# Kernel optimization log

Hardware: AMD Instinct MI355X
Metric: run time of the kernel (lower is better)

## Reference

```python
import jax, jax.numpy as jnp
import numpy as np

L = 3          # num_layers
D = 512        # hidden_dim
B, N = 8, 1024
EPS = 1e-5


def layernorm(x, gamma, beta):
    mu = jnp.mean(x, axis=-1, keepdims=True)
    var = jnp.var(x, axis=-1, keepdims=True)
    return (x - mu) * jax.lax.rsqrt(var + EPS) * gamma + beta


def setup_inputs() -> dict:
    key = jax.random.key(0)
    ks = jax.random.split(key, 12)
    s = 1.0 / np.sqrt(D)
    node_features = jax.random.normal(ks[0], (B, N, D), dtype=jnp.float32)
    adjacency_matrix = jax.random.randint(ks[1], (B, N, N), 0, 2, dtype=jnp.int32)
    return {
        "node_features": node_features,
        "adjacency_matrix": adjacency_matrix,
        # attn_linear: Linear(2D, 1) -> weight [2D], bias scalar, per layer
        "attn_w": jax.random.normal(ks[2], (L, 2 * D), dtype=jnp.float32) * (1.0 / np.sqrt(2 * D)),
        "attn_b": jax.random.normal(ks[3], (L,), dtype=jnp.float32) * 0.01,
        "W1": jax.random.normal(ks[4], (L, D, 4 * D), dtype=jnp.float32) * s,
        "b1": jnp.zeros((L, 4 * D), dtype=jnp.float32),
        "W2": jax.random.normal(ks[5], (L, 4 * D, D), dtype=jnp.float32) * (1.0 / np.sqrt(4 * D)),
        "b2": jnp.zeros((L, D), dtype=jnp.float32),
        "g1": jnp.ones((L, D), dtype=jnp.float32),
        "beta1": jnp.zeros((L, D), dtype=jnp.float32),
        "g2": jnp.ones((L, D), dtype=jnp.float32),
        "beta2": jnp.zeros((L, D), dtype=jnp.float32),
    }


def reference(node_features, adjacency_matrix, attn_w, attn_b, W1, b1, W2, b2, g1, beta1, g2, beta2):
    n = adjacency_matrix.shape[-1]
    # adjacency + self loops; mask of allowed edges
    mask = (adjacency_matrix.astype(jnp.float32) + jnp.eye(n, dtype=jnp.float32)) > 0  # [B,N,N]
    x = node_features
    d = x.shape[-1]
    for l in range(attn_w.shape[0]):
        # score_ij = a1.h_i + a2.h_j + b  (== Linear(concat(h_i,h_j)))
        si = x @ attn_w[l, :d]           # [B,N]
        sj = x @ attn_w[l, d:]           # [B,N]
        scores = si[:, :, None] + sj[:, None, :] + attn_b[l]   # [B,N,N]
        scores = jnp.where(scores >= 0, scores, 0.2 * scores)  # LeakyReLU(0.2)
        scores = jnp.where(mask, scores, -jnp.inf)
        attn = jax.nn.softmax(scores, axis=-1)                  # diag always unmasked
        agg = jnp.einsum('bij,bjd->bid', attn, x)
        h = layernorm(x + agg, g1[l], beta1[l])
        ff = jax.nn.gelu(h @ W1[l] + b1[l], approximate=False) @ W2[l] + b2[l]
        x = layernorm(h + ff, g2[l], beta2[l])
    return x
```

## Files before the change

### kernel.cpp

```cpp
#include <hip/hip_runtime.h>
#include <math.h>

#define NB 8
#define NN 1024
#define DD 512

typedef unsigned short u16;
typedef unsigned int u32;
typedef unsigned long long u64;
typedef __attribute__((ext_vector_type(8))) short bfrag;
typedef __attribute__((ext_vector_type(4))) float ffrag;

__device__ __forceinline__ u16 f2b(float f) {
    union { float f; u32 u; } v; v.f = f;
    u32 r = v.u + 0x7fffu + ((v.u >> 16) & 1u);
    return (u16)(r >> 16);
}
__device__ __forceinline__ float b2f(u16 b) {
    union { u32 u; float f; } v; v.u = ((u32)b) << 16;
    return v.f;
}

__device__ __forceinline__ float gelu_cheap(float v) {
    float s = v * 0.70710678118654752f;
    float a = fabsf(s);
    float t = 1.0f / (1.0f + 0.3275911f * a);
    float p = ((((1.061405429f * t - 1.453152027f) * t + 1.421413741f) * t
                - 0.284496736f) * t + 0.254829592f) * t;
    float erfa = 1.0f - p * __expf(-a * a);
    float erfs = copysignf(erfa, s);
    return 0.5f * v * (1.0f + erfs);
}

__device__ __forceinline__ void gload_lds16(const void* g, void* l) {
    __builtin_amdgcn_global_load_lds(
        (const __attribute__((address_space(1))) void*)g,
        (__attribute__((address_space(3))) void*)l, 16, 0, 0);
}

__global__ __launch_bounds__(256) void mask_pack(const int* __restrict__ adj,
                                                 u64* __restrict__ mb) {
    int idx = blockIdx.x * 256 + threadIdx.x;
    int w = idx & 15;
    int bi = idx >> 4;
    int i = bi & 1023;
    const int4* p = (const int4*)(adj + (size_t)bi * NN + w * 64);
    u64 m = 0;
#pragma unroll
    for (int q = 0; q < 16; ++q) {
        int4 v = p[q];
        if (v.x > 0) m |= 1ull << (q * 4 + 0);
        if (v.y > 0) m |= 1ull << (q * 4 + 1);
        if (v.z > 0) m |= 1ull << (q * 4 + 2);
        if (v.w > 0) m |= 1ull << (q * 4 + 3);
    }
    if (w == (i >> 6)) m |= 1ull << (i & 63);
    mb[idx] = m;
}

__global__ __launch_bounds__(256) void transpose_cvt(
    const float* __restrict__ in, u16* __restrict__ out,
    int R, int C, size_t inStr, size_t outStr)
{
    __shared__ float tile[32][33];
    int z = blockIdx.z;
    int r0 = blockIdx.y * 32, c0 = blockIdx.x * 32;
    int t = threadIdx.x;
    int tr = t >> 3, tc = (t & 7) * 4;
    float4 v = *(const float4*)(in + inStr * z + (size_t)(r0 + tr) * C + c0 + tc);
    tile[tr][tc + 0] = v.x; tile[tr][tc + 1] = v.y;
    tile[tr][tc + 2] = v.z; tile[tr][tc + 3] = v.w;
    __syncthreads();
    u32 w0 = (u32)f2b(tile[tc + 0][tr]) | ((u32)f2b(tile[tc + 1][tr]) << 16);
    u32 w1 = (u32)f2b(tile[tc + 2][tr]) | ((u32)f2b(tile[tc + 3][tr]) << 16);
    uint2 wv; wv.x = w0; wv.y = w1;
    *(uint2*)(out + outStr * z + (size_t)(c0 + tr) * R + r0 + tc) = wv;
}

__global__ __launch_bounds__(256) void score_proj_kernel(
    const float* __restrict__ x, const float* __restrict__ w,
    float* __restrict__ si, float* __restrict__ sj)
{
    int wave = threadIdx.x >> 6;
    int lane = threadIdx.x & 63;
    int row = blockIdx.x * 4 + wave;
    const float4* xr = (const float4*)(x + (size_t)row * DD) + lane * 2;
    const float4* w1 = (const float4*)(w) + lane * 2;
    const float4* w2 = (const float4*)(w + DD) + lane * 2;
    float a = 0.f, b2 = 0.f;
#pragma unroll
    for (int c = 0; c < 2; ++c) {
        float4 xv = xr[c], wa = w1[c], wb = w2[c];
        a  += xv.x * wa.x + xv.y * wa.y + xv.z * wa.z + xv.w * wa.w;
        b2 += xv.x * wb.x + xv.y * wb.y + xv.z * wb.z + xv.w * wb.w;
    }
#pragma unroll
    for (int off = 32; off > 0; off >>= 1) {
        a  += __shfl_xor(a, off);
        b2 += __shfl_xor(b2, off);
    }
    if (lane == 0) { si[row] = a; sj[row] = b2; }
}

__global__ __launch_bounds__(256) void softmax_p(
    const float* __restrict__ si, const float* __restrict__ sj,
    const float* __restrict__ attn_b, const u64* __restrict__ mb,
    u16* __restrict__ P)
{
    __shared__ u16 sb[8 * NN];
    int b  = blockIdx.x >> 7;
    int i0 = (blockIdx.x & 127) * 8;
    int tid = threadIdx.x;
    int r = tid >> 5, l32 = tid & 31;
    int i = i0 + r;
    float bb = attn_b[0];
    float siv = si[b * NN + i];
    const float* sjb = sj + b * NN;
    const u64* mbr = mb + ((size_t)b * NN + i) * 16;

    float sv[32];
    float mx = -INFINITY;
#pragma unroll
    for (int q = 0; q < 32; ++q) {
        int j = q * 32 + l32;
        u64 w = mbr[q >> 1];
        int bit = ((q & 1) << 5) + l32;
        float s = siv + sjb[j] + bb;
        s = (s >= 0.f) ? s : 0.2f * s;
        s = ((w >> bit) & 1ull) ? s : -INFINITY;
        sv[q] = s;
        mx = fmaxf(mx, s);
    }
#pragma unroll
    for (int off = 16; off > 0; off >>= 1) mx = fmaxf(mx, __shfl_xor(mx, off, 32));
    float sum = 0.f;
#pragma unroll
    for (int q = 0; q < 32; ++q) {
        float p = __expf(sv[q] - mx);
        sv[q] = p;
        sum += p;
    }
#pragma unroll
    for (int off = 16; off > 0; off >>= 1) sum += __shfl_xor(sum, off, 32);
    float inv = 1.f / sum;
#pragma unroll
    for (int q = 0; q < 32; ++q)
        sb[r * NN + q * 32 + l32] = f2b(sv[q] * inv);
    __syncthreads();
    const uint4* src = (const uint4*)sb;
    uint4* dst = (uint4*)(P + ((size_t)b * NN + i0) * NN);
#pragma unroll
    for (int t = 0; t < 4; ++t) dst[t * 256 + tid] = src[t * 256 + tid];
}

template <int EPI>
__global__ __launch_bounds__(256) void gemm64(
    const u16* __restrict__ A, const u16* __restrict__ Bm,
    const float* __restrict__ bias, const void* __restrict__ res,
    void* __restrict__ Cout, int K, int N, int lda, int ldb,
    size_t aStr, size_t bStr, size_t cStr, size_t resStr)
{
    __shared__ __align__(16) u16 lds[24576];
    int gx = gridDim.x, gy = gridDim.y;
    int wg = blockIdx.x + gx * (blockIdx.y + gy * blockIdx.z);
    int nwg = gx * gy * gridDim.z;
    wg = (wg & 7) * (nwg >> 3) + (wg >> 3);
    int z = wg / (gx * gy);
    int rem = wg - z * (gx * gy);
    int by = rem / gx, bx = rem - by * gx;
    int m0 = by * 64, n0 = bx * 128;
    int tid = threadIdx.x;
    int lane = tid & 63, wv = tid >> 6;

    const u16* ag[2]; const u16* bg[4];
    u32 la[2], lb[4];
#pragma unroll
    for (int i = 0; i < 2; ++i) {
        int q = i * 256 + tid;
        int row = q >> 3, c = q & 7;
        ag[i] = A + aStr * z + (size_t)(m0 + row) * lda + (c ^ (row & 7)) * 8;
        la[i] = i * 2048 + wv * 512;
    }
#pragma unroll
    for (int i = 0; i < 4; ++i) {
        int q = i * 256 + tid;
        int row = q >> 3, c = q & 7;
        bg[i] = Bm + bStr * z + (size_t)(n0 + row) * ldb + (c ^ (row & 7)) * 8;
        lb[i] = 8192 + i * 2048 + wv * 512;
    }

    int mw = (wv >> 1) * 32, nw = (wv & 1) * 64;
    int lr = lane & 15, lq = lane >> 4;
    int sw = lr & 7;

    ffrag acc[2][4];
#pragma unroll
    for (int i = 0; i < 2; ++i)
#pragma unroll
        for (int j = 0; j < 4; ++j) acc[i][j] = (ffrag){0.f, 0.f, 0.f, 0.f};

#pragma unroll
    for (int i = 0; i < 2; ++i) gload_lds16(ag[i], &lds[la[i]]);
#pragma unroll
    for (int i = 0; i < 4; ++i) gload_lds16(bg[i], &lds[lb[i]]);

    for (int k0 = 0; k0 < K; k0 += 64) {
        int cur = (k0 >> 6) & 1;
        if (k0 + 64 < K) {
#pragma unroll
            for (int i = 0; i < 2; ++i)
                gload_lds16(ag[i] + k0 + 64, &lds[((cur ^ 1) << 12) + la[i]]);
#pragma unroll
            for (int i = 0; i < 4; ++i)
                gload_lds16(bg[i] + k0 + 64, &lds[((cur ^ 1) << 13) + lb[i]]);
            asm volatile("s_waitcnt vmcnt(6)" ::: "memory");
        } else {
            asm volatile("s_waitcnt vmcnt(0)" ::: "memory");
        }
        asm volatile("s_barrier" ::: "memory");

        const u16* Ab = &lds[cur << 12];
        const u16* Bb = &lds[8192 + (cur << 13)];
#pragma unroll
        for (int h = 0; h < 2; ++h) {
            bfrag af[2], bf[4];
#pragma unroll
            for (int i = 0; i < 2; ++i)
                af[i] = *(const bfrag*)&Ab[(mw + i * 16 + lr) * 64 + ((h * 4 + lq) ^ sw) * 8];
#pragma unroll
            for (int j = 0; j < 4; ++j)
                bf[j] = *(const bfrag*)&Bb[(nw + j * 16 + lr) * 64 + ((h * 4 + lq) ^ sw) * 8];
#pragma unroll
            for (int i = 0; i < 2; ++i)
#pragma unroll
                for (int j = 0; j < 4; ++j)
                    acc[i][j] = __builtin_amdgcn_mfma_f32_16x16x32_bf16(af[i], bf[j], acc[i][j], 0, 0, 0);
        }
        asm volatile("s_waitcnt lgkmcnt(0)\ns_barrier" ::: "memory");
    }

    float* Cf = (float*)Cout + cStr * z;
    u16*   Cb = (u16*)Cout + cStr * z;
    const float* resf = (const float*)res;
    const u16*   resb = (const u16*)res;
#pragma unroll
    for (int i = 0; i < 2; ++i) {
        int row = m0 + mw + i * 16 + lq * 4;
#pragma unroll
        for (int j = 0; j < 4; ++j) {
            int col = n0 + nw + j * 16 + lr;
            float bv = (EPI != 0) ? bias[col] : 0.f;
#pragma unroll
            for (int r = 0; r < 4; ++r) {
                float v = acc[i][j][r] + bv;
                size_t off = (size_t)(row + r) * N + col;
                if (EPI == 1) {
                    Cb[off] = f2b(gelu_cheap(v));
                } else if (EPI == 0) {
                    Cf[off] = v + resf[resStr * z + off];
                } else {
                    Cf[off] = v + b2f(resb[off]);
                }
            }
        }
    }
}

template <int EPI>
__global__ __launch_bounds__(256) void gemm128(
    const u16* __restrict__ A, const u16* __restrict__ Bm,
    const float* __restrict__ bias, const void* __restrict__ res,
    void* __restrict__ Cout, int K, int N, int lda, int ldb,
    size_t aStr, size_t bStr, size_t cStr, size_t resStr)
{
    __shared__ __align__(16) u16 lds[32768];
    int gx = gridDim.x, gy = gridDim.y;
    int wg = blockIdx.x + gx * (blockIdx.y + gy * blockIdx.z);
    int nwg = gx * gy * gridDim.z;
    wg = (wg & 7) * (nwg >> 3) + (wg >> 3);
    int z = wg / (gx * gy);
    int rem = wg - z * (gx * gy);
    int by = rem / gx, bx = rem - by * gx;
    int m0 = by * 128, n0 = bx * 128;
    int tid = threadIdx.x;
    int lane = tid & 63, wv = tid >> 6;

    const u16* ag[4]; const u16* bg[4];
    u32 la[4], lb[4];
#pragma unroll
    for (int i = 0; i < 4; ++i) {
        int q = i * 256 + tid;
        int row = q >> 3, c = q & 7;
        ag[i] = A + aStr * z + (size_t)(m0 + row) * lda + (c ^ (row & 7)) * 8;
        la[i] = i * 2048 + wv * 512;
        bg[i] = Bm + bStr * z + (size_t)(n0 + row) * ldb + (c ^ (row & 7)) * 8;
        lb[i] = 16384 + i * 2048 + wv * 512;
    }

    int mw = (wv >> 1) * 64, nw = (wv & 1) * 64;
    int lr = lane & 15, lq = lane >> 4;
    int sw = lr & 7;

    ffrag acc[4][4];
#pragma unroll
    for (int i = 0; i < 4; ++i)
#pragma unroll
        for (int j = 0; j < 4; ++j) acc[i][j] = (ffrag){0.f, 0.f, 0.f, 0.f};

#pragma unroll
    for (int i = 0; i < 4; ++i) gload_lds16(ag[i], &lds[la[i]]);
#pragma unroll
    for (int i = 0; i < 4; ++i) gload_lds16(bg[i], &lds[lb[i]]);

    for (int k0 = 0; k0 < K; k0 += 64) {
        int cur = (k0 >> 6) & 1;
        if (k0 + 64 < K) {
#pragma unroll
            for (int i = 0; i < 4; ++i)
                gload_lds16(ag[i] + k0 + 64, &lds[((cur ^ 1) << 13) + la[i]]);
#pragma unroll
            for (int i = 0; i < 4; ++i)
                gload_lds16(bg[i] + k0 + 64, &lds[((cur ^ 1) << 13) + lb[i]]);
            asm volatile("s_waitcnt vmcnt(8)" ::: "memory");
        } else {
            asm volatile("s_waitcnt vmcnt(0)" ::: "memory");
        }
        asm volatile("s_barrier" ::: "memory");

        const u16* Ab = &lds[cur << 13];
        const u16* Bb = &lds[16384 + (cur << 13)];
#pragma unroll
        for (int h = 0; h < 2; ++h) {
            bfrag af[4], bf[4];
#pragma unroll
            for (int i = 0; i < 4; ++i)
                af[i] = *(const bfrag*)&Ab[(mw + i * 16 + lr) * 64 + ((h * 4 + lq) ^ sw) * 8];
#pragma unroll
            for (int j = 0; j < 4; ++j)
                bf[j] = *(const bfrag*)&Bb[(nw + j * 16 + lr) * 64 + ((h * 4 + lq) ^ sw) * 8];
#pragma unroll
            for (int i = 0; i < 4; ++i)
#pragma unroll
                for (int j = 0; j < 4; ++j)
                    acc[i][j] = __builtin_amdgcn_mfma_f32_16x16x32_bf16(af[i], bf[j], acc[i][j], 0, 0, 0);
        }
        asm volatile("s_waitcnt lgkmcnt(0)\ns_barrier" ::: "memory");
    }

    float* Cf = (float*)Cout + cStr * z;
    u16*   Cb = (u16*)Cout + cStr * z;
    const float* resf = (const float*)res;
    const u16*   resb = (const u16*)res;
    if (EPI == 1) {
        u16* sb = lds;
#pragma unroll
        for (int i = 0; i < 4; ++i) {
            int rr = mw + i * 16 + lq * 4;
#pragma unroll
            for (int j = 0; j < 4; ++j) {
                int cc = nw + j * 16 + lr;
                float bv = bias[n0 + cc];
#pragma unroll
                for (int r = 0; r < 4; ++r)
                    sb[(rr + r) * 136 + cc] = f2b(gelu_cheap(acc[i][j][r] + bv));
            }
        }
        __syncthreads();
        u16* Crow = Cb + (size_t)m0 * N + n0;
#pragma unroll
        for (int t = 0; t < 8; ++t) {
            int q = t * 256 + tid;
            int row = q >> 4, c16 = q & 15;
            *(uint4*)(Crow + (size_t)row * N + c16 * 8) =
                *(const uint4*)(sb + row * 136 + c16 * 8);
        }
    } else {
#pragma unroll
        for (int i = 0; i < 4; ++i) {
            int row = m0 + mw + i * 16 + lq * 4;
#pragma unroll
            for (int j = 0; j < 4; ++j) {
                int col = n0 + nw + j * 16 + lr;
                float bv = (EPI != 0) ? bias[col] : 0.f;
#pragma unroll
                for (int r = 0; r < 4; ++r) {
                    float v = acc[i][j][r] + bv;
                    size_t off = (size_t)(row + r) * N + col;
                    if (EPI == 0) {
                        Cf[off] = v + resf[resStr * z + off];
                    } else {
                        Cf[off] = v + b2f(resb[off]);
                    }
                }
            }
        }
    }
}

template <bool BF, bool SP>
__global__ __launch_bounds__(256) void ln_kernel(
    const float* __restrict__ in, const float* __restrict__ g,
    const float* __restrict__ be, void* __restrict__ out,
    const float* __restrict__ aw, float* __restrict__ si, float* __restrict__ sj)
{
    int row = blockIdx.x;
    int tid = threadIdx.x;
    const float2* rp = (const float2*)(in + (size_t)row * DD);
    float2 v = rp[tid];
    float s  = v.x + v.y;
    float ss = v.x * v.x + v.y * v.y;
#pragma unroll
    for (int off = 32; off > 0; off >>= 1) {
        s  += __shfl_xor(s, off);
        ss += __shfl_xor(ss, off);
    }
    __shared__ float sh[8];
    int wave = tid >> 6, lane = tid & 63;
    if (lane == 0) { sh[wave] = s; sh[4 + wave] = ss; }
    __syncthreads();
    float S  = sh[0] + sh[1] + sh[2] + sh[3];
    float SS = sh[4] + sh[5] + sh[6] + sh[7];
    float mean = S * (1.f / DD);
    float var  = SS * (1.f / DD) - mean * mean;
    var = fmaxf(var, 0.f);
    float rs = rsqrtf(var + 1e-5f);
    float2 gv = ((const float2*)g)[tid];
    float2 bv = ((const float2*)be)[tid];
    float ox = (v.x - mean) * rs * gv.x + bv.x;
    float oy = (v.y - mean) * rs * gv.y + bv.y;
    if (BF) {
        u32 w = (u32)f2b(ox) | ((u32)f2b(oy) << 16);
        ((u32*)out)[(size_t)row * (DD / 2) + tid] = w;
    } else {
        float2 o; o.x = ox; o.y = oy;
        ((float2*)out)[(size_t)row * (DD / 2) + tid] = o;
    }
    if (SP) {
        float2 wa = ((const float2*)aw)[tid];
        float2 wb = ((const float2*)(aw + DD))[tid];
        float a = ox * wa.x + oy * wa.y;
        float c = ox * wb.x + oy * wb.y;
#pragma unroll
        for (int off = 32; off > 0; off >>= 1) {
            a += __shfl_xor(a, off);
            c += __shfl_xor(c, off);
        }
        __syncthreads();
        if (lane == 0) { sh[wave] = a; sh[4 + wave] = c; }
        __syncthreads();
        if (tid == 0) {
            si[row] = sh[0] + sh[1] + sh[2] + sh[3];
            sj[row] = sh[4] + sh[5] + sh[6] + sh[7];
        }
    }
}

extern "C" void kernel_launch(void* const* d_in, const int* in_sizes, int n_in,
                              void* d_out, int out_size, void* d_ws, size_t ws_size,
                              hipStream_t stream) {
    const float* nf     = (const float*)d_in[0];
    const int*   adj    = (const int*)d_in[1];
    const float* attn_w = (const float*)d_in[2];
    const float* attn_b = (const float*)d_in[3];
    const float* W1     = (const float*)d_in[4];
    const float* b1     = (const float*)d_in[5];
    const float* W2     = (const float*)d_in[6];
    const float* b2     = (const float*)d_in[7];
    const float* g1     = (const float*)d_in[8];
    const float* be1    = (const float*)d_in[9];
    const float* g2     = (const float*)d_in[10];
    const float* be2    = (const float*)d_in[11];
    float* out = (float*)d_out;

    char* wsb = (char*)d_ws;
    float* x_cur = (float*)(wsb);
    u16*   h_bf  = (u16*)(wsb + 16777216);
    char*  scr   = wsb + 25165824;
    u16*   P     = (u16*)scr;
    float* hres  = (float*)(scr + 16777216);
    u16*   mid   = (u16*)scr;
    u16*   xT    = (u16*)(wsb + 58720256);
    u16*   W1t   = (u16*)(wsb + 67108864);
    u16*   W2t   = (u16*)(wsb + 73400320);
    u64*   mask  = (u64*)(wsb + 79691776);
    float* si    = (float*)(wsb + 80740352);
    float* sj    = (float*)(wsb + 80773120);

    mask_pack<<<512, 256, 0, stream>>>(adj, mask);
    transpose_cvt<<<dim3(64, 16, 3), 256, 0, stream>>>(W1, W1t, 512, 2048,
                                                       (size_t)512 * 2048, (size_t)512 * 2048);
    transpose_cvt<<<dim3(16, 64, 3), 256, 0, stream>>>(W2, W2t, 2048, 512,
                                                       (size_t)2048 * 512, (size_t)2048 * 512);

    score_proj_kernel<<<2048, 256, 0, stream>>>(nf, attn_w, si, sj);

    for (int l = 0; l < 3; ++l) {
        const float* xin = (l == 0) ? nf : x_cur;
        transpose_cvt<<<dim3(16, 32, 8), 256, 0, stream>>>(xin, xT, 1024, 512,
                                                           (size_t)NN * DD, (size_t)NN * DD);
        softmax_p<<<1024, 256, 0, stream>>>(si, sj, attn_b + l, mask, P);
        gemm64<0><<<dim3(4, 16, 8), 256, 0, stream>>>(
            P, xT, nullptr, xin, hres, 1024, 512, 1024, 1024,
            (size_t)NN * NN, (size_t)DD * NN, (size_t)NN * DD, (size_t)NN * DD);
        ln_kernel<true, false><<<8192, 256, 0, stream>>>(
            hres, g1 + (size_t)l * 512, be1 + (size_t)l * 512, h_bf, nullptr, nullptr, nullptr);
        gemm128<1><<<dim3(16, 64, 1), 256, 0, stream>>>(
            h_bf, W1t + (size_t)l * 1048576, b1 + (size_t)l * 2048, nullptr, mid,
            512, 2048, 512, 512, 0, 0, 0, 0);
        gemm64<2><<<dim3(4, 128, 1), 256, 0, stream>>>(
            mid, W2t + (size_t)l * 1048576, b2 + (size_t)l * 512, h_bf, x_cur,
            2048, 512, 2048, 2048, 0, 0, 0, 0);
        if (l < 2) {
            ln_kernel<false, true><<<8192, 256, 0, stream>>>(
                x_cur, g2 + (size_t)l * 512, be2 + (size_t)l * 512, x_cur,
                attn_w + (size_t)(l + 1) * 1024, si, sj);
        } else {
            ln_kernel<false, false><<<8192, 256, 0, stream>>>(
                x_cur, g2 + (size_t)l * 512, be2 + (size_t)l * 512, out,
                nullptr, nullptr, nullptr);
        }
    }
}
```

Before: 454.9 us.

## Fuse prep kernels and fold x transpose into LayerNorm epilogue

After: 482.8 us. +6.1%, slower.

```diff
diff --git a/kernel.cpp b/kernel.cpp
--- a/kernel.cpp
+++ b/kernel.cpp
@@ -38,68 +38,90 @@
         (__attribute__((address_space(3))) void*)l, 16, 0, 0);
 }
 
-__global__ __launch_bounds__(256) void mask_pack(const int* __restrict__ adj,
-                                                 u64* __restrict__ mb) {
-    int idx = blockIdx.x * 256 + threadIdx.x;
-    int w = idx & 15;
-    int bi = idx >> 4;
-    int i = bi & 1023;
-    const int4* p = (const int4*)(adj + (size_t)bi * NN + w * 64);
-    u64 m = 0;
-#pragma unroll
-    for (int q = 0; q < 16; ++q) {
-        int4 v = p[q];
-        if (v.x > 0) m |= 1ull << (q * 4 + 0);
-        if (v.y > 0) m |= 1ull << (q * 4 + 1);
-        if (v.z > 0) m |= 1ull << (q * 4 + 2);
-        if (v.w > 0) m |= 1ull << (q * 4 + 3);
-    }
-    if (w == (i >> 6)) m |= 1ull << (i & 63);
-    mb[idx] = m;
-}
-
-__global__ __launch_bounds__(256) void transpose_cvt(
+__device__ __forceinline__ void tcvt_body(
     const float* __restrict__ in, u16* __restrict__ out,
-    int R, int C, size_t inStr, size_t outStr)
-{
-    __shared__ float tile[32][33];
-    int z = blockIdx.z;
-    int r0 = blockIdx.y * 32, c0 = blockIdx.x * 32;
-    int t = threadIdx.x;
+    int R, int C, int r0, int c0, int t, float tile[32][33])
+{
     int tr = t >> 3, tc = (t & 7) * 4;
-    float4 v = *(const float4*)(in + inStr * z + (size_t)(r0 + tr) * C + c0 + tc);
+    float4 v = *(const float4*)(in + (size_t)(r0 + tr) * C + c0 + tc);
     tile[tr][tc + 0] = v.x; tile[tr][tc + 1] = v.y;
     tile[tr][tc + 2] = v.z; tile[tr][tc + 3] = v.w;
     __syncthreads();
     u32 w0 = (u32)f2b(tile[tc + 0][tr]) | ((u32)f2b(tile[tc + 1][tr]) << 16);
     u32 w1 = (u32)f2b(tile[tc + 2][tr]) | ((u32)f2b(tile[tc + 3][tr]) << 16);
     uint2 wv; wv.x = w0; wv.y = w1;
-    *(uint2*)(out + outStr * z + (size_t)(c0 + tr) * R + r0 + tc) = wv;
-}
-
-__global__ __launch_bounds__(256) void score_proj_kernel(
-    const float* __restrict__ x, const float* __restrict__ w,
-    float* __restrict__ si, float* __restrict__ sj)
-{
-    int wave = threadIdx.x >> 6;
-    int lane = threadIdx.x & 63;
-    int row = blockIdx.x * 4 + wave;
-    const float4* xr = (const float4*)(x + (size_t)row * DD) + lane * 2;
-    const float4* w1 = (const float4*)(w) + lane * 2;
-    const float4* w2 = (const float4*)(w + DD) + lane * 2;
-    float a = 0.f, b2 = 0.f;
-#pragma unroll
-    for (int c = 0; c < 2; ++c) {
-        float4 xv = xr[c], wa = w1[c], wb = w2[c];
-        a  += xv.x * wa.x + xv.y * wa.y + xv.z * wa.z + xv.w * wa.w;
-        b2 += xv.x * wb.x + xv.y * wb.y + xv.z * wb.z + xv.w * wb.w;
-    }
-#pragma unroll
-    for (int off = 32; off > 0; off >>= 1) {
-        a  += __shfl_xor(a, off);
-        b2 += __shfl_xor(b2, off);
-    }
-    if (lane == 0) { si[row] = a; sj[row] = b2; }
+    *(uint2*)(out + (size_t)(c0 + tr) * R + r0 + tc) = wv;
+}
+
+__global__ __launch_bounds__(256) void prep_fused(
+    const int* __restrict__ adj, u64* __restrict__ mb,
+    const float* __restrict__ nf, const float* __restrict__ attn_w,
+    float* __restrict__ si, float* __restrict__ sj, u16* __restrict__ xT)
+{
+    __shared__ float tile[32][33];
+    int bid = blockIdx.x;
+    int tid = threadIdx.x;
+    if (bid < 512) {
+        int idx = bid * 256 + tid;
+        int w = idx & 15;
+        int bi = idx >> 4;
+        int i = bi & 1023;
+        const int4* p = (const int4*)(adj + (size_t)bi * NN + w * 64);
+        u64 m = 0;
+#pragma unroll
+        for (int q = 0; q < 16; ++q) {
+            int4 v = p[q];
+            if (v.x > 0) m |= 1ull << (q * 4 + 0);
+            if (v.y > 0) m |= 1ull << (q * 4 + 1);
+            if (v.z > 0) m |= 1ull << (q * 4 + 2);
+            if (v.w > 0) m |= 1ull << (q * 4 + 3);
+        }
+        if (w == (i >> 6)) m |= 1ull << (i & 63);
+        mb[idx] = m;
+    } else if (bid < 2560) {
+        int wave = tid >> 6;
+        int lane = tid & 63;
+        int row = (bid - 512) * 4 + wave;
+        const float4* xr = (const float4*)(nf + (size_t)row * DD) + lane * 2;
+        const float4* w1 = (const float4*)(attn_w) + lane * 2;
+        const float4* w2 = (const float4*)(attn_w + DD) + lane * 2;
+        float a = 0.f, b2 = 0.f;
+#pragma unroll
+        for (int c = 0; c < 2; ++c) {
+            float4 xv = xr[c], wa = w1[c], wb = w2[c];
+            a  += xv.x * wa.x + xv.y * wa.y + xv.z * wa.z + xv.w * wa.w;
+            b2 += xv.x * wb.x + xv.y * wb.y + xv.z * wb.z + xv.w * wb.w;
+        }
+#pragma unroll
+        for (int off = 32; off > 0; off >>= 1) {
+            a  += __shfl_xor(a, off);
+            b2 += __shfl_xor(b2, off);
+        }
+        if (lane == 0) { si[row] = a; sj[row] = b2; }
+    } else {
+        int q = bid - 2560;
+        int bx = q & 15, by = (q >> 4) & 31, bz = q >> 9;
+        tcvt_body(nf + (size_t)bz * NN * DD, xT + (size_t)bz * NN * DD,
+                  1024, 512, by * 32, bx * 32, tid, tile);
+    }
+}
+
+__global__ __launch_bounds__(256) void trans_w(
+    const float* __restrict__ W1, const float* __restrict__ W2,
+    u16* __restrict__ W1t, u16* __restrict__ W2t)
+{
+    __shared__ float tile[32][33];
+    int z = blockIdx.z;
+    int bx = blockIdx.x, by = blockIdx.y;
+    if (z < 3) {
+        tcvt_body(W1 + (size_t)z * 512 * 2048, W1t + (size_t)z * 1048576,
+                  512, 2048, by * 32, bx * 32, threadIdx.x, tile);
+    } else {
+        int q = by * 64 + bx;
+        int bx2 = q & 15, by2 = q >> 4;
+        tcvt_body(W2 + (size_t)(z - 3) * 2048 * 512, W2t + (size_t)(z - 3) * 1048576,
+                  2048, 512, by2 * 32, bx2 * 32, threadIdx.x, tile);
+    }
 }
 
 __global__ __launch_bounds__(256) void softmax_p(
@@ -240,7 +262,6 @@
     }
 
     float* Cf = (float*)Cout + cStr * z;
-    u16*   Cb = (u16*)Cout + cStr * z;
     const float* resf = (const float*)res;
     const u16*   resb = (const u16*)res;
 #pragma unroll
@@ -254,9 +275,7 @@
             for (int r = 0; r < 4; ++r) {
                 float v = acc[i][j][r] + bv;
                 size_t off = (size_t)(row + r) * N + col;
-                if (EPI == 1) {
-                    Cb[off] = f2b(gelu_cheap(v));
-                } else if (EPI == 0) {
+                if (EPI == 0) {
                     Cf[off] = v + resf[resStr * z + off];
                 } else {
                     Cf[off] = v + b2f(resb[off]);
@@ -397,60 +416,88 @@
     }
 }
 
-template <bool BF, bool SP>
-__global__ __launch_bounds__(256) void ln_kernel(
+template <bool BF, bool SP, bool XT>
+__global__ __launch_bounds__(256) void ln32_kernel(
     const float* __restrict__ in, const float* __restrict__ g,
     const float* __restrict__ be, void* __restrict__ out,
-    const float* __restrict__ aw, float* __restrict__ si, float* __restrict__ sj)
-{
-    int row = blockIdx.x;
+    const float* __restrict__ aw, float* __restrict__ si, float* __restrict__ sj,
+    u16* __restrict__ xT)
+{
+    __shared__ __align__(16) u16 tp[XT ? 512 * 40 : 8];
+    int row0 = blockIdx.x * 32;
     int tid = threadIdx.x;
-    const float2* rp = (const float2*)(in + (size_t)row * DD);
-    float2 v = rp[tid];
-    float s  = v.x + v.y;
-    float ss = v.x * v.x + v.y * v.y;
-#pragma unroll
-    for (int off = 32; off > 0; off >>= 1) {
+    int r = tid >> 3, sub = tid & 7;
+    int row = row0 + r;
+    const float4* rp = (const float4*)(in + (size_t)row * DD) + sub * 16;
+    float4 v[16];
+    float s = 0.f, ss = 0.f;
+#pragma unroll
+    for (int q = 0; q < 16; ++q) {
+        float4 t = rp[q]; v[q] = t;
+        s  += t.x + t.y + t.z + t.w;
+        ss += t.x * t.x + t.y * t.y + t.z * t.z + t.w * t.w;
+    }
+#pragma unroll
+    for (int off = 1; off < 8; off <<= 1) {
         s  += __shfl_xor(s, off);
         ss += __shfl_xor(ss, off);
     }
-    __shared__ float sh[8];
-    int wave = tid >> 6, lane = tid & 63;
-    if (lane == 0) { sh[wave] = s; sh[4 + wave] = ss; }
-    __syncthreads();
-    float S  = sh[0] + sh[1] + sh[2] + sh[3];
-    float SS = sh[4] + sh[5] + sh[6] + sh[7];
-    float mean = S * (1.f / DD);
-    float var  = SS * (1.f / DD) - mean * mean;
+    float mean = s * (1.f / DD);
+    float var  = ss * (1.f / DD) - mean * mean;
     var = fmaxf(var, 0.f);
     float rs = rsqrtf(var + 1e-5f);
-    float2 gv = ((const float2*)g)[tid];
-    float2 bv = ((const float2*)be)[tid];
-    float ox = (v.x - mean) * rs * gv.x + bv.x;
-    float oy = (v.y - mean) * rs * gv.y + bv.y;
-    if (BF) {
-        u32 w = (u32)f2b(ox) | ((u32)f2b(oy) << 16);
-        ((u32*)out)[(size_t)row * (DD / 2) + tid] = w;
-    } else {
-        float2 o; o.x = ox; o.y = oy;
-        ((float2*)out)[(size_t)row * (DD / 2) + tid] = o;
+    const float4* gp = (const float4*)g  + sub * 16;
+    const float4* bp = (const float4*)be + sub * 16;
+    const float4* wap = (const float4*)aw + sub * 16;
+    const float4* wbp = (const float4*)(aw + DD) + sub * 16;
+    float a = 0.f, c2 = 0.f;
+#pragma unroll
+    for (int q = 0; q < 16; ++q) {
+        float4 gv = gp[q], bv = bp[q], t = v[q];
+        float4 o;
+        o.x = (t.x - mean) * rs * gv.x + bv.x;
+        o.y = (t.y - mean) * rs * gv.y + bv.y;
+        o.z = (t.z - mean) * rs * gv.z + bv.z;
+        o.w = (t.w - mean) * rs * gv.w + bv.w;
+        if (BF) {
+            uint2 wv2;
+            wv2.x = (u32)f2b(o.x) | ((u32)f2b(o.y) << 16);
+            wv2.y = (u32)f2b(o.z) | ((u32)f2b(o.w) << 16);
+            ((uint2*)out)[(size_t)row * 128 + sub * 16 + q] = wv2;
+        } else {
+            ((float4*)out)[(size_t)row * 128 + sub * 16 + q] = o;
+        }
+        if (SP) {
+            float4 wa = wap[q], wb = wbp[q];
+            a  += o.x * wa.x + o.y * wa.y + o.z * wa.z + o.w * wa.w;
+            c2 += o.x * wb.x + o.y * wb.y + o.z * wb.z + o.w * wb.w;
+        }
+        if (XT) {
+            int c = sub * 64 + q * 4;
+            tp[(c + 0) * 40 + r] = f2b(o.x);
+            tp[(c + 1) * 40 + r] = f2b(o.y);
+            tp[(c + 2) * 40 + r] = f2b(o.z);
+            tp[(c + 3) * 40 + r] = f2b(o.w);
+        }
     }
     if (SP) {
-        float2 wa = ((const float2*)aw)[tid];
-        float2 wb = ((const float2*)(aw + DD))[tid];
-        float a = ox * wa.x + oy * wa.y;
-        float c = ox * wb.x + oy * wb.y;
-#pragma unroll
-        for (int off = 32; off > 0; off >>= 1) {
-            a += __shfl_xor(a, off);
-            c += __shfl_xor(c, off);
-        }
+#pragma unroll
+        for (int off = 1; off < 8; off <<= 1) {
+            a  += __shfl_xor(a, off);
+            c2 += __shfl_xor(c2, off);
+        }
+        if (sub == 0) { si[row] = a; sj[row] = c2; }
+    }
+    if (XT) {
         __syncthreads();
-        if (lane == 0) { sh[wave] = a; sh[4 + wave] = c; }
-        __syncthreads();
-        if (tid == 0) {
-            si[row] = sh[0] + sh[1] + sh[2] + sh[3];
-            sj[row] = sh[4] + sh[5] + sh[6] + sh[7];
+        int b = row0 >> 10, i0 = row0 & 1023;
+        u16* xb = xT + (size_t)b * (512 * 1024) + i0;
+#pragma unroll
+        for (int t2 = 0; t2 < 8; ++t2) {
+            int q2 = t2 * 256 + tid;
+            int d = q2 >> 2, c16 = q2 & 3;
+            *(uint4*)(xb + (size_t)d * 1024 + c16 * 8) =
+                *(const uint4*)(tp + d * 40 + c16 * 8);
         }
     }
 }
@@ -486,24 +533,18 @@
     float* si    = (float*)(wsb + 80740352);
     float* sj    = (float*)(wsb + 80773120);
 
-    mask_pack<<<512, 256, 0, stream>>>(adj, mask);
-    transpose_cvt<<<dim3(64, 16, 3), 256, 0, stream>>>(W1, W1t, 512, 2048,
-                                                       (size_t)512 * 2048, (size_t)512 * 2048);
-    transpose_cvt<<<dim3(16, 64, 3), 256, 0, stream>>>(W2, W2t, 2048, 512,
-                                                       (size_t)2048 * 512, (size_t)2048 * 512);
-
-    score_proj_kernel<<<2048, 256, 0, stream>>>(nf, attn_w, si, sj);
+    prep_fused<<<6656, 256, 0, stream>>>(adj, mask, nf, attn_w, si, sj, xT);
+    trans_w<<<dim3(64, 16, 6), 256, 0, stream>>>(W1, W2, W1t, W2t);
 
     for (int l = 0; l < 3; ++l) {
         const float* xin = (l == 0) ? nf : x_cur;
-        transpose_cvt<<<dim3(16, 32, 8), 256, 0, stream>>>(xin, xT, 1024, 512,
-                                                           (size_t)NN * DD, (size_t)NN * DD);
         softmax_p<<<1024, 256, 0, stream>>>(si, sj, attn_b + l, mask, P);
         gemm64<0><<<dim3(4, 16, 8), 256, 0, stream>>>(
             P, xT, nullptr, xin, hres, 1024, 512, 1024, 1024,
             (size_t)NN * NN, (size_t)DD * NN, (size_t)NN * DD, (size_t)NN * DD);
-        ln_kernel<true, false><<<8192, 256, 0, stream>>>(
-            hres, g1 + (size_t)l * 512, be1 + (size_t)l * 512, h_bf, nullptr, nullptr, nullptr);
+        ln32_kernel<true, false, false><<<256, 256, 0, stream>>>(
+            hres, g1 + (size_t)l * 512, be1 + (size_t)l * 512, h_bf,
+            attn_w, nullptr, nullptr, nullptr);
         gemm128<1><<<dim3(16, 64, 1), 256, 0, stream>>>(
             h_bf, W1t + (size_t)l * 1048576, b1 + (size_t)l * 2048, nullptr, mid,
             512, 2048, 512, 512, 0, 0, 0, 0);
@@ -511,13 +552,13 @@
             mid, W2t + (size_t)l * 1048576, b2 + (size_t)l * 512, h_bf, x_cur,
             2048, 512, 2048, 2048, 0, 0, 0, 0);
         if (l < 2) {
-            ln_kernel<false, true><<<8192, 256, 0, stream>>>(
+            ln32_kernel<false, true, true><<<256, 256, 0, stream>>>(
                 x_cur, g2 + (size_t)l * 512, be2 + (size_t)l * 512, x_cur,
-                attn_w + (size_t)(l + 1) * 1024, si, sj);
+                attn_w + (size_t)(l + 1) * 1024, si, sj, xT);
         } else {
-            ln_kernel<false, false><<<8192, 256, 0, stream>>>(
+            ln32_kernel<false, false, false><<<256, 256, 0, stream>>>(
                 x_cur, g2 + (size_t)l * 512, be2 + (size_t)l * 512, out,
-                nullptr, nullptr, nullptr);
-        }
-    }
-}
+                attn_w, nullptr, nullptr, nullptr);
+        }
+    }
+}
```
